# Kernel optimization log

Measured on AMD Instinct MI355X. Metric: run time of the kernel, lower is better.

## Reference

```python
import jax, jax.numpy as jnp
import numpy as np

B, QL, SL = 8, 1024, 2048
Q_IN, QK, KV_IN, VD, OUT = 1024, 512, 1024, 512, 1024
NEG = -1e10


def setup_inputs() -> dict:
    key = jax.random.key(0)
    ks = jax.random.split(key, 12)
    init = lambda k, shp, fan: jax.random.uniform(k, shp, jnp.float32, -1.0, 1.0) / np.sqrt(fan)
    return {
        "q": jax.random.normal(ks[0], (B, QL, Q_IN), jnp.float32),
        "s": jax.random.normal(ks[1], (B, SL, KV_IN), jnp.float32),
        "mask": jax.random.randint(ks[2], (B, 1, SL), 0, 2, jnp.int32),
        "Wq": init(ks[3], (Q_IN, QK), Q_IN),
        "bq": init(ks[4], (QK,), Q_IN),
        "Wk": init(ks[5], (KV_IN, QK), KV_IN),
        "bk": init(ks[6], (QK,), KV_IN),
        "Wv": init(ks[7], (KV_IN, VD), KV_IN),
        "bv": init(ks[8], (VD,), KV_IN),
        "Wo": init(ks[9], (VD, OUT), VD),
        "bo": init(ks[10], (OUT,), VD),
    }


def reference(q, s, mask, Wq, bq, Wk, bk, Wv, bv, Wo, bo):
    qp = q @ Wq + bq            # [B, QL, QK]
    k = s @ Wk + bk             # [B, SL, QK]
    v = s @ Wv + bv             # [B, SL, VD]
    scale = jnp.asarray(QK ** 0.5, qp.dtype)
    score = jnp.einsum("bqh,bsh->bqs", qp, k) / scale
    score = jnp.where(mask == 0, jnp.asarray(NEG, score.dtype), score)
    attn_w = jax.nn.softmax(score, axis=-1)          # [B, QL, SL]
    attn_out = jnp.einsum("bqs,bsh->bqh", attn_w, v)  # [B, QL, VD]
    attn_out = attn_out @ Wo + bo                     # [B, QL, OUT]
    return attn_w, attn_out
```

## Files before the change

### kernel.cpp

```cpp
#include <hip/hip_runtime.h>
#include <stdint.h>

static constexpr int B_   = 8;
static constexpr int QL   = 1024;
static constexpr int SLEN = 2048;
static constexpr int QIN  = 1024;
static constexpr int QKD  = 512;
static constexpr int KVIN = 1024;
static constexpr int VDIM = 512;
static constexpr int OUTD = 1024;

typedef float  f32x4  __attribute__((ext_vector_type(4)));
typedef __bf16 bf16x8 __attribute__((ext_vector_type(8)));
typedef unsigned short u16x8 __attribute__((ext_vector_type(8)));

__device__ __forceinline__ unsigned short f2bf(float f) {
  unsigned int u = __builtin_bit_cast(unsigned int, f);
  return (unsigned short)((u + 0x7FFFu + ((u >> 16) & 1u)) >> 16);
}

__device__ __forceinline__ void async16(const void* g, void* l) {
  __builtin_amdgcn_global_load_lds(
      (__attribute__((address_space(1))) void*)(uintptr_t)g,
      (__attribute__((address_space(3))) void*)(unsigned int)(uintptr_t)l,
      16, 0, 0);
}

template<int EPI>
__global__ __launch_bounds__(256) void gemm_bt_k(
    const unsigned short* __restrict__ Ap, const unsigned short* __restrict__ Btp,
    const float* __restrict__ bias, void* __restrict__ Cp,
    int N, int K, long sA, long sB, long sC,
    const int* __restrict__ maskp, float scale)
{
  __shared__ unsigned short tA[128 * 32];
  __shared__ unsigned short tB[128 * 32];

  const unsigned gx = gridDim.x, gy = gridDim.y;
  const unsigned nwg = gx * gy * gridDim.z;
  const unsigned orig = blockIdx.x + gx * (blockIdx.y + gy * blockIdx.z);
  const unsigned swz = (orig & 7) * (nwg >> 3) + (orig >> 3);
  const unsigned bx = swz % gx;
  const unsigned rem = swz / gx;
  const unsigned by = rem % gy;
  const unsigned z  = rem / gy;

  const int tid  = threadIdx.x;
  const int wave = tid >> 6, lane = tid & 63;
  const int wr = wave >> 1, wc = wave & 1;
  const int fr = lane & 15, fq = lane >> 4;
  const int row0 = by * 128, col0 = bx * 128;

  const unsigned short* A  = Ap  + (size_t)z * sA;
  const unsigned short* Bt = Btp + (size_t)z * sB;

  f32x4 acc[4][4];
#pragma unroll
  for (int i = 0; i < 4; ++i)
#pragma unroll
    for (int j = 0; j < 4; ++j) acc[i][j] = (f32x4)0.f;

  const int r_st  = (wave << 5) + (lane >> 2);
  const int k_off = (lane & 3) << 3;

  const int nk = K >> 5;
  for (int kt = 0; kt < nk; ++kt) {
    __syncthreads();
    const int kbase = kt << 5;
#pragma unroll
    for (int c = 0; c < 2; ++c) {
      const int r = r_st + (c << 4);
      async16(Bt + (size_t)(col0 + r) * K + kbase + k_off, &tB[(wave << 10) + (c << 9)]);
      async16(A  + (size_t)(row0 + r) * K + kbase + k_off, &tA[(wave << 10) + (c << 9)]);
    }
    __syncthreads();

    bf16x8 af[4], bfv[4];
#pragma unroll
    for (int mi = 0; mi < 4; ++mi)
      af[mi] = __builtin_bit_cast(bf16x8,
                 *(const u16x8*)&tA[((wr << 6) + (mi << 4) + fr) * 32 + (fq << 3)]);
#pragma unroll
    for (int ni = 0; ni < 4; ++ni)
      bfv[ni] = __builtin_bit_cast(bf16x8,
                 *(const u16x8*)&tB[((wc << 6) + (ni << 4) + fr) * 32 + (fq << 3)]);
#pragma unroll
    for (int mi = 0; mi < 4; ++mi)
#pragma unroll
      for (int ni = 0; ni < 4; ++ni)
        acc[mi][ni] = __builtin_amdgcn_mfma_f32_16x16x32_bf16(af[mi], bfv[ni], acc[mi][ni], 0, 0, 0);
  }

#pragma unroll
  for (int mi = 0; mi < 4; ++mi) {
#pragma unroll
    for (int ni = 0; ni < 4; ++ni) {
      const int col = col0 + (wc << 6) + (ni << 4) + fr;
      const float bval = (EPI == 1) ? 0.f : (bias ? bias[col] : 0.f);
#pragma unroll
      for (int j = 0; j < 4; ++j) {
        const int row = row0 + (wr << 6) + (mi << 4) + (fq << 2) + j;
        const float v = acc[mi][ni][j];
        if constexpr (EPI == 0) {
          ((unsigned short*)Cp)[(size_t)z * sC + (size_t)row * N + col] = f2bf(v + bval);
        } else if constexpr (EPI == 1) {
          float o = maskp[(size_t)z * SLEN + col] ? v * scale : -1e10f;
          ((float*)Cp)[(size_t)z * sC + (size_t)row * N + col] = o;
        } else {
          ((float*)Cp)[(size_t)z * sC + (size_t)row * N + col] = v + bval;
        }
      }
    }
  }
}

__global__ __launch_bounds__(256) void cvt_k(const float* __restrict__ in,
                                             unsigned short* __restrict__ out)
{
  const size_t i = ((size_t)blockIdx.x * 256 + threadIdx.x) * 8;
  float4 a = *(const float4*)(in + i), b = *(const float4*)(in + i + 4);
  u16x8 o;
  o[0]=f2bf(a.x); o[1]=f2bf(a.y); o[2]=f2bf(a.z); o[3]=f2bf(a.w);
  o[4]=f2bf(b.x); o[5]=f2bf(b.y); o[6]=f2bf(b.z); o[7]=f2bf(b.w);
  *(u16x8*)(out + i) = o;
}

__global__ __launch_bounds__(256) void tcvt_k(const float* __restrict__ in, int R, int C,
                                              unsigned short* __restrict__ out)
{
  __shared__ unsigned short t[64][65];
  const int c0 = blockIdx.x << 6, r0 = blockIdx.y << 6;
#pragma unroll
  for (int p = 0; p < 16; ++p) {
    int idx = threadIdx.x + (p << 8);
    int i = idx >> 6, j = idx & 63;
    t[i][j] = f2bf(in[(size_t)(r0 + i) * C + c0 + j]);
  }
  __syncthreads();
#pragma unroll
  for (int p = 0; p < 16; ++p) {
    int idx = threadIdx.x + (p << 8);
    int jj = idx >> 6, ii = idx & 63;
    out[(size_t)(c0 + jj) * R + r0 + ii] = t[ii][jj];
  }
}

__global__ __launch_bounds__(256) void vtrans_k(const unsigned short* __restrict__ v,
                                                unsigned short* __restrict__ vt)
{
  __shared__ unsigned short t[64][72];
  const int b  = blockIdx.z;
  const int v0 = blockIdx.x << 6;
  const int s0 = blockIdx.y << 6;
  const unsigned short* src = v + ((size_t)b * SLEN + s0) * VDIM + v0;
#pragma unroll
  for (int p = 0; p < 2; ++p) {
    int idx = threadIdx.x + (p << 8);
    int i = idx >> 3, j8 = (idx & 7) << 3;
    *(u16x8*)&t[i][j8] = *(const u16x8*)&src[(size_t)i * VDIM + j8];
  }
  __syncthreads();
  unsigned short* dst = vt + ((size_t)b * VDIM + v0) * SLEN + s0;
#pragma unroll
  for (int p = 0; p < 2; ++p) {
    int idx = threadIdx.x + (p << 8);
    int jj = idx >> 3, i8 = (idx & 7) << 3;
    u16x8 o;
#pragma unroll
    for (int e = 0; e < 8; ++e) o[e] = t[i8 + e][jj];
    *(u16x8*)&dst[(size_t)jj * SLEN + i8] = o;
  }
}

__global__ __launch_bounds__(256) void softmax_k(float* __restrict__ p,
                                                 unsigned short* __restrict__ pb)
{
  __shared__ float red[8];
  const size_t base = (size_t)blockIdx.x * SLEN;
  const int t = threadIdx.x;
  float4* p4 = (float4*)(p + base);
  float4 a = p4[t * 2], b = p4[t * 2 + 1];

  float m = fmaxf(fmaxf(fmaxf(a.x, a.y), fmaxf(a.z, a.w)),
                  fmaxf(fmaxf(b.x, b.y), fmaxf(b.z, b.w)));
#pragma unroll
  for (int off = 32; off >= 1; off >>= 1) m = fmaxf(m, __shfl_xor(m, off));
  const int wave = t >> 6, lane = t & 63;
  if (lane == 0) red[wave] = m;
  __syncthreads();
  m = fmaxf(fmaxf(red[0], red[1]), fmaxf(red[2], red[3]));

  a.x = __expf(a.x - m); a.y = __expf(a.y - m); a.z = __expf(a.z - m); a.w = __expf(a.w - m);
  b.x = __expf(b.x - m); b.y = __expf(b.y - m); b.z = __expf(b.z - m); b.w = __expf(b.w - m);
  float sum = a.x + a.y + a.z + a.w + b.x + b.y + b.z + b.w;
#pragma unroll
  for (int off = 32; off >= 1; off >>= 1) sum += __shfl_xor(sum, off);
  if (lane == 0) red[4 + wave] = sum;
  __syncthreads();
  const float inv = 1.f / (red[4] + red[5] + red[6] + red[7]);

  a.x *= inv; a.y *= inv; a.z *= inv; a.w *= inv;
  b.x *= inv; b.y *= inv; b.z *= inv; b.w *= inv;
  p4[t * 2] = a; p4[t * 2 + 1] = b;

  u16x8 o;
  o[0]=f2bf(a.x); o[1]=f2bf(a.y); o[2]=f2bf(a.z); o[3]=f2bf(a.w);
  o[4]=f2bf(b.x); o[5]=f2bf(b.y); o[6]=f2bf(b.z); o[7]=f2bf(b.w);
  *(u16x8*)(pb + base + (size_t)t * 8) = o;
}

extern "C" void kernel_launch(void* const* d_in, const int* in_sizes, int n_in,
                              void* d_out, int out_size, void* d_ws, size_t ws_size,
                              hipStream_t stream)
{
  const float* q  = (const float*)d_in[0];
  const float* s  = (const float*)d_in[1];
  const int* mask = (const int*)d_in[2];
  const float* Wq = (const float*)d_in[3];
  const float* bq = (const float*)d_in[4];
  const float* Wk = (const float*)d_in[5];
  const float* bk = (const float*)d_in[6];
  const float* Wv = (const float*)d_in[7];
  const float* bv = (const float*)d_in[8];
  const float* Wo = (const float*)d_in[9];
  const float* bo = (const float*)d_in[10];

  char* ws = (char*)d_ws;
  unsigned short* WqT = (unsigned short*)(ws + ((size_t)0  << 20));
  unsigned short* WkT = (unsigned short*)(ws + ((size_t)1  << 20));
  unsigned short* WvT = (unsigned short*)(ws + ((size_t)2  << 20));
  unsigned short* WoT = (unsigned short*)(ws + ((size_t)3  << 20));
  unsigned short* qbf = (unsigned short*)(ws + ((size_t)4  << 20));
  unsigned short* vbf = qbf;
  unsigned short* sbf = (unsigned short*)(ws + ((size_t)20 << 20));
  unsigned short* pw  = sbf;
  unsigned short* qp  = (unsigned short*)(ws + ((size_t)52 << 20));
  unsigned short* ao  = qp;
  unsigned short* kb  = (unsigned short*)(ws + ((size_t)60 << 20));
  unsigned short* vT  = (unsigned short*)(ws + ((size_t)76 << 20));

  float* attn_w = (float*)d_out;
  float* attn_o = (float*)d_out + (size_t)B_ * QL * SLEN;

  cvt_k<<<(B_ * QL * QIN) / (256 * 8), 256, 0, stream>>>(q, qbf);
  cvt_k<<<(B_ * SLEN * KVIN) / (256 * 8), 256, 0, stream>>>(s, sbf);
  tcvt_k<<<dim3(QKD / 64, QIN / 64),   256, 0, stream>>>(Wq, QIN,  QKD,  WqT);
  tcvt_k<<<dim3(QKD / 64, KVIN / 64),  256, 0, stream>>>(Wk, KVIN, QKD,  WkT);
  tcvt_k<<<dim3(VDIM / 64, KVIN / 64), 256, 0, stream>>>(Wv, KVIN, VDIM, WvT);
  tcvt_k<<<dim3(OUTD / 64, VDIM / 64), 256, 0, stream>>>(Wo, VDIM, OUTD, WoT);

  gemm_bt_k<0><<<dim3(QKD / 128, (B_ * QL) / 128), 256, 0, stream>>>(
      qbf, WqT, bq, qp, QKD, QIN, 0, 0, 0, nullptr, 0.f);
  gemm_bt_k<0><<<dim3(QKD / 128, (B_ * SLEN) / 128), 256, 0, stream>>>(
      sbf, WkT, bk, kb, QKD, KVIN, 0, 0, 0, nullptr, 0.f);
  gemm_bt_k<0><<<dim3(VDIM / 128, (B_ * SLEN) / 128), 256, 0, stream>>>(
      sbf, WvT, bv, vbf, VDIM, KVIN, 0, 0, 0, nullptr, 0.f);

  vtrans_k<<<dim3(VDIM / 64, SLEN / 64, B_), 256, 0, stream>>>(vbf, vT);

  gemm_bt_k<1><<<dim3(SLEN / 128, QL / 128, B_), 256, 0, stream>>>(
      qp, kb, nullptr, attn_w, SLEN, QKD,
      (long)QL * QKD, (long)SLEN * QKD, (long)QL * SLEN, mask, 0.044194173824159216f);

  softmax_k<<<B_ * QL, 256, 0, stream>>>(attn_w, pw);

  gemm_bt_k<0><<<dim3(VDIM / 128, QL / 128, B_), 256, 0, stream>>>(
      pw, vT, nullptr, ao, VDIM, SLEN,
      (long)QL * SLEN, (long)VDIM * SLEN, (long)QL * VDIM, nullptr, 0.f);

  gemm_bt_k<2><<<dim3(OUTD / 128, (B_ * QL) / 128), 256, 0, stream>>>(
      ao, WoT, bo, attn_o, OUTD, VDIM, 0, 0, 0, nullptr, 0.f);
}
```

Measured before the change: 424.9 us.

## Double-buffer GEMM K-tiles, fuse K/V projections, and store scores in bf16

The GEMM kernel now stages 64-wide K tiles into double-buffered LDS, prefetching the next tile while MFMAs run on the current one, with one barrier per iteration. The K and V projections are merged into a single GEMM over concatenated weights and biases. The score GEMM writes bf16 scores instead of fp32, and softmax reads those and writes both the fp32 weights and the bf16 probabilities in place. This cuts launches and score-matrix traffic, but rounds pre-softmax scores to bf16, which loses precision, and the larger LDS footprint may lower occupancy.

```diff
diff --git a/kernel.cpp b/kernel.cpp
--- a/kernel.cpp
+++ b/kernel.cpp
@@ -18,6 +18,9 @@
   unsigned int u = __builtin_bit_cast(unsigned int, f);
   return (unsigned short)((u + 0x7FFFu + ((u >> 16) & 1u)) >> 16);
 }
+__device__ __forceinline__ float bf2f(unsigned short h) {
+  return __builtin_bit_cast(float, (unsigned int)h << 16);
+}
 
 __device__ __forceinline__ void async16(const void* g, void* l) {
   __builtin_amdgcn_global_load_lds(
@@ -30,11 +33,11 @@
 __global__ __launch_bounds__(256) void gemm_bt_k(
     const unsigned short* __restrict__ Ap, const unsigned short* __restrict__ Btp,
     const float* __restrict__ bias, void* __restrict__ Cp,
-    int N, int K, long sA, long sB, long sC,
+    int K, int ldA, int ldB, int ldC,
+    long sA, long sB, long sC,
     const int* __restrict__ maskp, float scale)
 {
-  __shared__ unsigned short tA[128 * 32];
-  __shared__ unsigned short tB[128 * 32];
+  __shared__ unsigned short lds[4][128 * 64];
 
   const unsigned gx = gridDim.x, gy = gridDim.y;
   const unsigned nwg = gx * gy * gridDim.z;
@@ -60,35 +63,54 @@
 #pragma unroll
     for (int j = 0; j < 4; ++j) acc[i][j] = (f32x4)0.f;
 
-  const int r_st  = (wave << 5) + (lane >> 2);
-  const int k_off = (lane & 3) << 3;
-
-  const int nk = K >> 5;
+  const int s_r   = tid >> 3;
+  const int s_k   = (tid & 7) << 3;
+  const int s_lds = (wave << 9);
+  auto stage = [&](const unsigned short* G, int ld, int g0, int kbase,
+                   unsigned short* buf) {
+#pragma unroll
+    for (int c = 0; c < 4; ++c) {
+      async16(G + (size_t)(g0 + (c << 5) + s_r) * ld + kbase + s_k,
+              buf + (c << 11) + s_lds);
+    }
+  };
+
+  const int nk = K >> 6;
+  stage(A,  ldA, row0, 0, lds[0]);
+  stage(Bt, ldB, col0, 0, lds[1]);
+  __syncthreads();
+
+  int cur = 0;
   for (int kt = 0; kt < nk; ++kt) {
+    if (kt + 1 < nk) {
+      const int kb2 = (kt + 1) << 6;
+      stage(A,  ldA, row0, kb2, lds[((cur ^ 1) << 1)]);
+      stage(Bt, ldB, col0, kb2, lds[((cur ^ 1) << 1) | 1]);
+    }
+    const unsigned short* tAc = lds[(cur << 1)];
+    const unsigned short* tBc = lds[(cur << 1) | 1];
+
+    bf16x8 af[2][4], bfv[2][4];
+#pragma unroll
+    for (int ks = 0; ks < 2; ++ks) {
+#pragma unroll
+      for (int mi = 0; mi < 4; ++mi)
+        af[ks][mi] = __builtin_bit_cast(bf16x8,
+            *(const u16x8*)&tAc[((wr << 6) + (mi << 4) + fr) * 64 + (ks << 5) + (fq << 3)]);
+#pragma unroll
+      for (int ni = 0; ni < 4; ++ni)
+        bfv[ks][ni] = __builtin_bit_cast(bf16x8,
+            *(const u16x8*)&tBc[((wc << 6) + (ni << 4) + fr) * 64 + (ks << 5) + (fq << 3)]);
+    }
+#pragma unroll
+    for (int mi = 0; mi < 4; ++mi)
+#pragma unroll
+      for (int ni = 0; ni < 4; ++ni) {
+        acc[mi][ni] = __builtin_amdgcn_mfma_f32_16x16x32_bf16(af[0][mi], bfv[0][ni], acc[mi][ni], 0, 0, 0);
+        acc[mi][ni] = __builtin_amdgcn_mfma_f32_16x16x32_bf16(af[1][mi], bfv[1][ni], acc[mi][ni], 0, 0, 0);
+      }
     __syncthreads();
-    const int kbase = kt << 5;
-#pragma unroll
-    for (int c = 0; c < 2; ++c) {
-      const int r = r_st + (c << 4);
-      async16(Bt + (size_t)(col0 + r) * K + kbase + k_off, &tB[(wave << 10) + (c << 9)]);
-      async16(A  + (size_t)(row0 + r) * K + kbase + k_off, &tA[(wave << 10) + (c << 9)]);
-    }
-    __syncthreads();
-
-    bf16x8 af[4], bfv[4];
-#pragma unroll
-    for (int mi = 0; mi < 4; ++mi)
-      af[mi] = __builtin_bit_cast(bf16x8,
-                 *(const u16x8*)&tA[((wr << 6) + (mi << 4) + fr) * 32 + (fq << 3)]);
-#pragma unroll
-    for (int ni = 0; ni < 4; ++ni)
-      bfv[ni] = __builtin_bit_cast(bf16x8,
-                 *(const u16x8*)&tB[((wc << 6) + (ni << 4) + fr) * 32 + (fq << 3)]);
-#pragma unroll
-    for (int mi = 0; mi < 4; ++mi)
-#pragma unroll
-      for (int ni = 0; ni < 4; ++ni)
-        acc[mi][ni] = __builtin_amdgcn_mfma_f32_16x16x32_bf16(af[mi], bfv[ni], acc[mi][ni], 0, 0, 0);
+    cur ^= 1;
   }
 
 #pragma unroll
@@ -102,12 +124,12 @@
         const int row = row0 + (wr << 6) + (mi << 4) + (fq << 2) + j;
         const float v = acc[mi][ni][j];
         if constexpr (EPI == 0) {
-          ((unsigned short*)Cp)[(size_t)z * sC + (size_t)row * N + col] = f2bf(v + bval);
+          ((unsigned short*)Cp)[(size_t)z * sC + (size_t)row * ldC + col] = f2bf(v + bval);
         } else if constexpr (EPI == 1) {
           float o = maskp[(size_t)z * SLEN + col] ? v * scale : -1e10f;
-          ((float*)Cp)[(size_t)z * sC + (size_t)row * N + col] = o;
+          ((unsigned short*)Cp)[(size_t)z * sC + (size_t)row * ldC + col] = f2bf(o);
         } else {
-          ((float*)Cp)[(size_t)z * sC + (size_t)row * N + col] = v + bval;
+          ((float*)Cp)[(size_t)z * sC + (size_t)row * ldC + col] = v + bval;
         }
       }
     }
@@ -145,19 +167,28 @@
   }
 }
 
+__global__ __launch_bounds__(256) void catbias_k(const float* __restrict__ a,
+                                                 const float* __restrict__ b,
+                                                 float* __restrict__ o)
+{
+  int i = blockIdx.x * 256 + threadIdx.x;
+  o[i] = (i < 512) ? a[i] : b[i - 512];
+}
+
 __global__ __launch_bounds__(256) void vtrans_k(const unsigned short* __restrict__ v,
+                                                int ldv,
                                                 unsigned short* __restrict__ vt)
 {
   __shared__ unsigned short t[64][72];
   const int b  = blockIdx.z;
   const int v0 = blockIdx.x << 6;
   const int s0 = blockIdx.y << 6;
-  const unsigned short* src = v + ((size_t)b * SLEN + s0) * VDIM + v0;
+  const unsigned short* src = v + ((size_t)b * SLEN + s0) * ldv + v0;
 #pragma unroll
   for (int p = 0; p < 2; ++p) {
     int idx = threadIdx.x + (p << 8);
     int i = idx >> 3, j8 = (idx & 7) << 3;
-    *(u16x8*)&t[i][j8] = *(const u16x8*)&src[(size_t)i * VDIM + j8];
+    *(u16x8*)&t[i][j8] = *(const u16x8*)&src[(size_t)i * ldv + j8];
   }
   __syncthreads();
   unsigned short* dst = vt + ((size_t)b * VDIM + v0) * SLEN + s0;
@@ -172,17 +203,20 @@
   }
 }
 
-__global__ __launch_bounds__(256) void softmax_k(float* __restrict__ p,
-                                                 unsigned short* __restrict__ pb)
+__global__ __launch_bounds__(256) void softmax_k(unsigned short* __restrict__ sc,
+                                                 float* __restrict__ wf)
 {
   __shared__ float red[8];
   const size_t base = (size_t)blockIdx.x * SLEN;
   const int t = threadIdx.x;
-  float4* p4 = (float4*)(p + base);
-  float4 a = p4[t * 2], b = p4[t * 2 + 1];
-
-  float m = fmaxf(fmaxf(fmaxf(a.x, a.y), fmaxf(a.z, a.w)),
-                  fmaxf(fmaxf(b.x, b.y), fmaxf(b.z, b.w)));
+  u16x8 r = *(const u16x8*)(sc + base + (size_t)t * 8);
+  float x[8];
+#pragma unroll
+  for (int e = 0; e < 8; ++e) x[e] = bf2f(r[e]);
+
+  float m = x[0];
+#pragma unroll
+  for (int e = 1; e < 8; ++e) m = fmaxf(m, x[e]);
 #pragma unroll
   for (int off = 32; off >= 1; off >>= 1) m = fmaxf(m, __shfl_xor(m, off));
   const int wave = t >> 6, lane = t & 63;
@@ -190,23 +224,24 @@
   __syncthreads();
   m = fmaxf(fmaxf(red[0], red[1]), fmaxf(red[2], red[3]));
 
-  a.x = __expf(a.x - m); a.y = __expf(a.y - m); a.z = __expf(a.z - m); a.w = __expf(a.w - m);
-  b.x = __expf(b.x - m); b.y = __expf(b.y - m); b.z = __expf(b.z - m); b.w = __expf(b.w - m);
-  float sum = a.x + a.y + a.z + a.w + b.x + b.y + b.z + b.w;
+  float sum = 0.f;
+#pragma unroll
+  for (int e = 0; e < 8; ++e) { x[e] = __expf(x[e] - m); sum += x[e]; }
 #pragma unroll
   for (int off = 32; off >= 1; off >>= 1) sum += __shfl_xor(sum, off);
   if (lane == 0) red[4 + wave] = sum;
   __syncthreads();
   const float inv = 1.f / (red[4] + red[5] + red[6] + red[7]);
 
-  a.x *= inv; a.y *= inv; a.z *= inv; a.w *= inv;
-  b.x *= inv; b.y *= inv; b.z *= inv; b.w *= inv;
-  p4[t * 2] = a; p4[t * 2 + 1] = b;
-
-  u16x8 o;
-  o[0]=f2bf(a.x); o[1]=f2bf(a.y); o[2]=f2bf(a.z); o[3]=f2bf(a.w);
-  o[4]=f2bf(b.x); o[5]=f2bf(b.y); o[6]=f2bf(b.z); o[7]=f2bf(b.w);
-  *(u16x8*)(pb + base + (size_t)t * 8) = o;
+#pragma unroll
+  for (int e = 0; e < 8; ++e) x[e] *= inv;
+  float4 o0 = {x[0], x[1], x[2], x[3]}, o1 = {x[4], x[5], x[6], x[7]};
+  *(float4*)(wf + base + (size_t)t * 8)     = o0;
+  *(float4*)(wf + base + (size_t)t * 8 + 4) = o1;
+  u16x8 ob;
+#pragma unroll
+  for (int e = 0; e < 8; ++e) ob[e] = f2bf(x[e]);
+  *(u16x8*)(sc + base + (size_t)t * 8) = ob;
 }
 
 extern "C" void kernel_launch(void* const* d_in, const int* in_sizes, int n_in,
@@ -226,18 +261,17 @@
   const float* bo = (const float*)d_in[10];
 
   char* ws = (char*)d_ws;
-  unsigned short* WqT = (unsigned short*)(ws + ((size_t)0  << 20));
-  unsigned short* WkT = (unsigned short*)(ws + ((size_t)1  << 20));
-  unsigned short* WvT = (unsigned short*)(ws + ((size_t)2  << 20));
-  unsigned short* WoT = (unsigned short*)(ws + ((size_t)3  << 20));
-  unsigned short* qbf = (unsigned short*)(ws + ((size_t)4  << 20));
-  unsigned short* vbf = qbf;
-  unsigned short* sbf = (unsigned short*)(ws + ((size_t)20 << 20));
-  unsigned short* pw  = sbf;
-  unsigned short* qp  = (unsigned short*)(ws + ((size_t)52 << 20));
-  unsigned short* ao  = qp;
-  unsigned short* kb  = (unsigned short*)(ws + ((size_t)60 << 20));
-  unsigned short* vT  = (unsigned short*)(ws + ((size_t)76 << 20));
+  unsigned short* WqT  = (unsigned short*)(ws + ((size_t)0  << 20));
+  unsigned short* WkvT = (unsigned short*)(ws + ((size_t)1  << 20));
+  unsigned short* WoT  = (unsigned short*)(ws + ((size_t)3  << 20));
+  unsigned short* qbf  = (unsigned short*)(ws + ((size_t)4  << 20));
+  unsigned short* sbf  = (unsigned short*)(ws + ((size_t)20 << 20));
+  unsigned short* sc   = sbf;
+  unsigned short* qp   = (unsigned short*)(ws + ((size_t)52 << 20));
+  unsigned short* ao   = qp;
+  unsigned short* kv   = (unsigned short*)(ws + ((size_t)60 << 20));
+  unsigned short* vT   = (unsigned short*)(ws + ((size_t)92 << 20));
+  float*          bkv  = (float*)         (ws + ((size_t)108 << 20));
 
   float* attn_w = (float*)d_out;
   float* attn_o = (float*)d_out + (size_t)B_ * QL * SLEN;
@@ -245,29 +279,28 @@
   cvt_k<<<(B_ * QL * QIN) / (256 * 8), 256, 0, stream>>>(q, qbf);
   cvt_k<<<(B_ * SLEN * KVIN) / (256 * 8), 256, 0, stream>>>(s, sbf);
   tcvt_k<<<dim3(QKD / 64, QIN / 64),   256, 0, stream>>>(Wq, QIN,  QKD,  WqT);
-  tcvt_k<<<dim3(QKD / 64, KVIN / 64),  256, 0, stream>>>(Wk, KVIN, QKD,  WkT);
-  tcvt_k<<<dim3(VDIM / 64, KVIN / 64), 256, 0, stream>>>(Wv, KVIN, VDIM, WvT);
+  tcvt_k<<<dim3(QKD / 64, KVIN / 64),  256, 0, stream>>>(Wk, KVIN, QKD,  WkvT);
+  tcvt_k<<<dim3(VDIM / 64, KVIN / 64), 256, 0, stream>>>(Wv, KVIN, VDIM, WkvT + (size_t)QKD * KVIN);
   tcvt_k<<<dim3(OUTD / 64, VDIM / 64), 256, 0, stream>>>(Wo, VDIM, OUTD, WoT);
+  catbias_k<<<4, 256, 0, stream>>>(bk, bv, bkv);
 
   gemm_bt_k<0><<<dim3(QKD / 128, (B_ * QL) / 128), 256, 0, stream>>>(
-      qbf, WqT, bq, qp, QKD, QIN, 0, 0, 0, nullptr, 0.f);
-  gemm_bt_k<0><<<dim3(QKD / 128, (B_ * SLEN) / 128), 256, 0, stream>>>(
-      sbf, WkT, bk, kb, QKD, KVIN, 0, 0, 0, nullptr, 0.f);
-  gemm_bt_k<0><<<dim3(VDIM / 128, (B_ * SLEN) / 128), 256, 0, stream>>>(
-      sbf, WvT, bv, vbf, VDIM, KVIN, 0, 0, 0, nullptr, 0.f);
-
-  vtrans_k<<<dim3(VDIM / 64, SLEN / 64, B_), 256, 0, stream>>>(vbf, vT);
+      qbf, WqT, bq, qp, QIN, QIN, QIN, QKD, 0, 0, 0, nullptr, 0.f);
+  gemm_bt_k<0><<<dim3((QKD + VDIM) / 128, (B_ * SLEN) / 128), 256, 0, stream>>>(
+      sbf, WkvT, bkv, kv, KVIN, KVIN, KVIN, QKD + VDIM, 0, 0, 0, nullptr, 0.f);
+
+  vtrans_k<<<dim3(VDIM / 64, SLEN / 64, B_), 256, 0, stream>>>(kv + QKD, QKD + VDIM, vT);
 
   gemm_bt_k<1><<<dim3(SLEN / 128, QL / 128, B_), 256, 0, stream>>>(
-      qp, kb, nullptr, attn_w, SLEN, QKD,
-      (long)QL * QKD, (long)SLEN * QKD, (long)QL * SLEN, mask, 0.044194173824159216f);
-
-  softmax_k<<<B_ * QL, 256, 0, stream>>>(attn_w, pw);
+      qp, kv, nullptr, sc, QKD, QKD, QKD + VDIM, SLEN,
+      (long)QL * QKD, (long)SLEN * (QKD + VDIM), (long)QL * SLEN, mask, 0.044194173824159216f);
+
+  softmax_k<<<B_ * QL, 256, 0, stream>>>(sc, attn_w);
 
   gemm_bt_k<0><<<dim3(VDIM / 128, QL / 128, B_), 256, 0, stream>>>(
-      pw, vT, nullptr, ao, VDIM, SLEN,
+      sc, vT, nullptr, ao, SLEN, SLEN, SLEN, VDIM,
       (long)QL * SLEN, (long)VDIM * SLEN, (long)QL * VDIM, nullptr, 0.f);
 
   gemm_bt_k<2><<<dim3(OUTD / 128, (B_ * QL) / 128), 256, 0, stream>>>(
-      ao, WoT, bo, attn_o, OUTD, VDIM, 0, 0, 0, nullptr, 0.f);
-}
+      ao, WoT, bo, attn_o, VDIM, VDIM, VDIM, OUTD, 0, 0, 0, nullptr, 0.f);
+}
```

New measurement: 373.2 us. 1.14x faster.
